# Performance work log

Hardware: AMD Instinct MI355X
Metric: run time of the kernel (lower is better)

Reference implementation:

```python
import jax, jax.numpy as jnp
import numpy as np

TAU = 1.0      # temperature for gumbel-softmax
EPS = 1e-12    # F.normalize eps


def _l2norm(v, axis):
    n = jnp.sqrt(jnp.sum(v * v, axis=axis, keepdims=True))
    return v / jnp.maximum(n, EPS)


def setup_inputs() -> dict:
    key = jax.random.key(0)
    k1, k2, k3, k4 = jax.random.split(key, 4)
    b, c, h, w, n = 8, 512, 64, 64, 1024
    x = jax.random.normal(k1, (b, c, h, w), dtype=jnp.float32)
    centers = jax.random.normal(k2, (n, c), dtype=jnp.float32)          # VQ codebook
    clusters = jax.random.normal(k3, (n, c), dtype=jnp.float32)         # ClusterLookup param
    gumbel_noise = jax.random.gumbel(k4, (b, n, h, w), dtype=jnp.float32)
    return {"x": x, "centers": centers, "clusters": clusters, "gumbel_noise": gumbel_noise}


def reference(x, centers, clusters, gumbel_noise):
    # similarity logits: [b, n, h, w]
    inner = jnp.einsum('bchw,nc->bnhw', x, centers)
    # hard gumbel-softmax (straight-through) over code dim
    y_soft = jax.nn.softmax((inner + gumbel_noise) / TAU, axis=1)
    idx = jnp.argmax(y_soft, axis=1)                                     # [b, h, w]
    y_hard = jax.nn.one_hot(idx, centers.shape[0], axis=1, dtype=y_soft.dtype)
    one_hot = y_hard - jax.lax.stop_gradient(y_soft) + y_soft            # [b, n, h, w]
    # quantized features: codebook lookup expressed as einsum
    z_q = jnp.einsum('bnhw,nd->bdhw', one_hot, centers)                  # [b, c, h, w]
    # ClusterLookup(z_q, alpha=None, is_direct=False)
    nf = _l2norm(z_q, axis=1)
    ncl = _l2norm(clusters, axis=1)
    ip = jnp.einsum('bchw,nc->bnhw', nf, ncl)                            # cluster logits
    preds = jnp.argmax(ip, axis=1)                                       # [b, h, w] int
    probs = jax.nn.one_hot(preds, clusters.shape[0], axis=1, dtype=ip.dtype)
    cluster_loss = -jnp.mean(jnp.sum(probs * ip, axis=1))
    return (cluster_loss, preds, ip, z_q)
```

## Files before the change

### kernel.cpp

```cpp
#include <hip/hip_runtime.h>
#include <math.h>

#define C 512
#define HW 4096
#define N 1024
#define NPIX 32768
#define MARGIN 2.0f

typedef short s16x8 __attribute__((ext_vector_type(8)));
typedef float f32x4 __attribute__((ext_vector_type(4)));

__device__ inline unsigned short f2bf(float f) {
    unsigned int u = __float_as_uint(f);
    return (unsigned short)((u + 0x7FFFu + ((u >> 16) & 1u)) >> 16);
}
__device__ inline float h2f(unsigned short u) {
    _Float16 h; __builtin_memcpy(&h, &u, 2); return (float)h;
}
__device__ inline unsigned short f2h(float f) {
    _Float16 h = (_Float16)f; unsigned short u; __builtin_memcpy(&u, &h, 2); return u;
}
__device__ inline unsigned int mono(float v) {
    unsigned int u = __float_as_uint(v);
    return (u & 0x80000000u) ? ~u : (u | 0x80000000u);
}

__global__ __launch_bounds__(64) void k_norms(const float* __restrict__ centers,
                                              const float* __restrict__ clusters,
                                              float* __restrict__ cnorm,
                                              float* __restrict__ clnorm) {
    int r = blockIdx.x;
    const float* src = (r < N) ? (centers + (size_t)r * C) : (clusters + (size_t)(r - N) * C);
    int lane = threadIdx.x;
    float s = 0.f;
    for (int k = lane; k < C; k += 64) { float v = src[k]; s += v * v; }
    #pragma unroll
    for (int m = 1; m < 64; m <<= 1) s += __shfl_xor(s, m, 64);
    if (lane == 0) {
        float nrm = sqrtf(s);
        if (nrm < 1e-12f) nrm = 1e-12f;
        if (r < N) cnorm[r] = nrm; else clnorm[r - N] = nrm;
    }
}

__global__ __launch_bounds__(256) void k_gemmM(const float* __restrict__ centers,
                                               const float* __restrict__ clusters,
                                               const float* __restrict__ cnorm,
                                               const float* __restrict__ clnorm,
                                               float* __restrict__ M) {
    __shared__ float as[32][68];
    __shared__ float bs[32][68];
    int tid = threadIdx.x;
    int tx = tid & 15, ty = tid >> 4;
    int i0 = blockIdx.x * 64, j0 = blockIdx.y * 64;
    int lrow = tid >> 2, lkq = (tid & 3) * 8;
    float acc[4][4] = {};
    for (int kc = 0; kc < C; kc += 32) {
        float4 a0 = *(const float4*)(centers + (size_t)(i0 + lrow) * C + kc + lkq);
        float4 a1 = *(const float4*)(centers + (size_t)(i0 + lrow) * C + kc + lkq + 4);
        float4 b0 = *(const float4*)(clusters + (size_t)(j0 + lrow) * C + kc + lkq);
        float4 b1 = *(const float4*)(clusters + (size_t)(j0 + lrow) * C + kc + lkq + 4);
        __syncthreads();
        as[lkq+0][lrow]=a0.x; as[lkq+1][lrow]=a0.y; as[lkq+2][lrow]=a0.z; as[lkq+3][lrow]=a0.w;
        as[lkq+4][lrow]=a1.x; as[lkq+5][lrow]=a1.y; as[lkq+6][lrow]=a1.z; as[lkq+7][lrow]=a1.w;
        bs[lkq+0][lrow]=b0.x; bs[lkq+1][lrow]=b0.y; bs[lkq+2][lrow]=b0.z; bs[lkq+3][lrow]=b0.w;
        bs[lkq+4][lrow]=b1.x; bs[lkq+5][lrow]=b1.y; bs[lkq+6][lrow]=b1.z; bs[lkq+7][lrow]=b1.w;
        __syncthreads();
        #pragma unroll
        for (int k = 0; k < 32; k += 4) {
            float av[4][4], bv[4][4];
            #pragma unroll
            for (int kk = 0; kk < 4; ++kk) {
                float4 ta = *(const float4*)&as[k+kk][tx*4];
                float4 tb = *(const float4*)&bs[k+kk][ty*4];
                av[kk][0]=ta.x; av[kk][1]=ta.y; av[kk][2]=ta.z; av[kk][3]=ta.w;
                bv[kk][0]=tb.x; bv[kk][1]=tb.y; bv[kk][2]=tb.z; bv[kk][3]=tb.w;
            }
            #pragma unroll
            for (int kk = 0; kk < 4; ++kk)
                #pragma unroll
                for (int ii = 0; ii < 4; ++ii)
                    #pragma unroll
                    for (int jj = 0; jj < 4; ++jj)
                        acc[ii][jj] = fmaf(av[kk][ii], bv[kk][jj], acc[ii][jj]);
        }
    }
    float rci[4], rcj[4];
    #pragma unroll
    for (int ii = 0; ii < 4; ++ii) rci[ii] = cnorm[i0 + tx*4 + ii];
    #pragma unroll
    for (int jj = 0; jj < 4; ++jj) rcj[jj] = clnorm[j0 + ty*4 + jj];
    #pragma unroll
    for (int ii = 0; ii < 4; ++ii)
        #pragma unroll
        for (int jj = 0; jj < 4; ++jj)
            M[(size_t)(i0 + tx*4 + ii) * N + (j0 + ty*4 + jj)] = acc[ii][jj] / (rci[ii] * rcj[jj]);
}

__global__ __launch_bounds__(256) void k_rowstat(const float* __restrict__ M,
                                                 float* __restrict__ rowmax,
                                                 int* __restrict__ rowarg) {
    __shared__ float sv[256];
    __shared__ int   sa[256];
    int i = blockIdx.x, tid = threadIdx.x;
    float bv = -INFINITY; int ba = 0;
    for (int j = tid; j < N; j += 256) {
        float v = M[(size_t)i * N + j];
        if (v > bv || (v == bv && j < ba)) { bv = v; ba = j; }
    }
    sv[tid] = bv; sa[tid] = ba;
    __syncthreads();
    for (int s = 128; s > 0; s >>= 1) {
        if (tid < s) {
            float v = sv[tid + s]; int a = sa[tid + s];
            if (v > sv[tid] || (v == sv[tid] && a < sa[tid])) { sv[tid] = v; sa[tid] = a; }
        }
        __syncthreads();
    }
    if (tid == 0) { rowmax[i] = sv[0]; rowarg[i] = sa[0]; }
}

__global__ __launch_bounds__(256) void k_prepT(const float* __restrict__ x,
                                               float* __restrict__ xT) {
    __shared__ float t[64][65];
    int bidx = blockIdx.x;
    int pt = bidx & 63, kt = (bidx >> 6) & 7, b = bidx >> 9;
    int r = threadIdx.x >> 4, c4 = (threadIdx.x & 15) * 4;
    const float* src = x + ((size_t)b * C + kt * 64) * HW + pt * 64;
    #pragma unroll
    for (int rr = 0; rr < 4; ++rr) {
        int row = rr * 16 + r;
        float4 v = *(const float4*)(src + (size_t)row * HW + c4);
        t[row][c4] = v.x; t[row][c4+1] = v.y; t[row][c4+2] = v.z; t[row][c4+3] = v.w;
    }
    __syncthreads();
    float* dst = xT + ((size_t)b * HW + pt * 64) * C + kt * 64;
    #pragma unroll
    for (int rr = 0; rr < 4; ++rr) {
        int row = rr * 16 + r;
        float4 v = { t[c4][row], t[c4+1][row], t[c4+2][row], t[c4+3][row] };
        *(float4*)(dst + (size_t)row * C + c4) = v;
    }
}

__global__ __launch_bounds__(64) void k_cenfrag(const float* __restrict__ centers,
                                                unsigned short* __restrict__ cenB) {
    int f = blockIdx.x;
    int nt = f >> 4, kt = f & 15;
    int lane = threadIdx.x;
    int r = lane & 15, g = lane >> 4;
    const float* src = centers + (size_t)(nt * 16 + r) * C + kt * 32 + g * 4;
    float4 lo = *(const float4*)src;
    float4 hi = *(const float4*)(src + 16);
    union { unsigned short us[8]; uint4 q; } u;
    u.us[0]=f2bf(lo.x); u.us[1]=f2bf(lo.y); u.us[2]=f2bf(lo.z); u.us[3]=f2bf(lo.w);
    u.us[4]=f2bf(hi.x); u.us[5]=f2bf(hi.y); u.us[6]=f2bf(hi.z); u.us[7]=f2bf(hi.w);
    *(uint4*)(cenB + ((size_t)f * 64 + lane) * 8) = u.q;
}

__global__ __launch_bounds__(512, 4) void k_fused(const float* __restrict__ xT,
                                                  const unsigned short* __restrict__ cenB,
                                                  const float* __restrict__ gumbel,
                                                  const float* __restrict__ centers,
                                                  int* __restrict__ idxb) {
    __shared__ uint4 cen4[2][2][1024];
    __shared__ unsigned long long pixkey[64];
    __shared__ unsigned int candlist[8][256];
    __shared__ int candcount[8];

    int tid = threadIdx.x;
    int lane = tid & 63, w = tid >> 6;
    int r = lane & 15, g = lane >> 4;
    int pt = w & 3, gr = w >> 2;

    int p0 = blockIdx.x * 64;
    int b = p0 >> 12, hw0 = p0 & (HW - 1);

    if (tid < 64) pixkey[tid] = 0ull;
    if (tid < 8) candcount[tid] = 0;

    s16x8 a[16];
    {
        const float* xrow = xT + (size_t)(p0 + pt * 16 + r) * C;
        #pragma unroll
        for (int kt = 0; kt < 16; ++kt) {
            float4 lo = *(const float4*)(xrow + kt * 32 + g * 4);
            float4 hi = *(const float4*)(xrow + kt * 32 + 16 + g * 4);
            s16x8 t;
            t[0]=(short)f2bf(lo.x); t[1]=(short)f2bf(lo.y); t[2]=(short)f2bf(lo.z); t[3]=(short)f2bf(lo.w);
            t[4]=(short)f2bf(hi.x); t[5]=(short)f2bf(hi.y); t[6]=(short)f2bf(hi.z); t[7]=(short)f2bf(hi.w);
            a[kt] = t;
        }
    }

    const uint4* cb = (const uint4*)cenB;
    {
        const uint4* src = cb + (size_t)(gr * 32) * 1024 + pt * 256 + lane;
        uint4* dst = &cen4[gr][0][pt * 256 + lane];
        #pragma unroll
        for (int i = 0; i < 4; ++i) dst[i * 64] = src[i * 64];
    }
    __syncthreads();

    float m4[4] = {-INFINITY, -INFINITY, -INFINITY, -INFINITY};
    int cur = 0;
    const float* gpx = gumbel + (size_t)b * N * HW + hw0 + pt * 16 + g * 4;

    for (int tc = 0; tc < 8; ++tc) {
        unsigned int keepH[8];
        #pragma unroll
        for (int s = 0; s < 4; ++s) {
            int t = tc * 4 + s;
            int tn = t + 1;
            uint4 cr0, cr1, cr2, cr3;
            if (tn < 32) {
                const uint4* src = cb + (size_t)(gr * 32 + tn) * 1024 + pt * 256 + lane;
                cr0 = src[0]; cr1 = src[64]; cr2 = src[128]; cr3 = src[192];
            }
            float4 gv = *(const float4*)(gpx + (size_t)((gr * 32 + t) * 16 + r) * HW);
            const s16x8* bp = (const s16x8*)&cen4[gr][cur][0] + lane;
            f32x4 acc0 = {0.f,0.f,0.f,0.f}, acc1 = {0.f,0.f,0.f,0.f};
            #pragma unroll
            for (int kt = 0; kt < 16; kt += 2) {
                acc0 = __builtin_amdgcn_mfma_f32_16x16x32_bf16(a[kt],   bp[kt*64],     acc0, 0,0,0);
                acc1 = __builtin_amdgcn_mfma_f32_16x16x32_bf16(a[kt+1], bp[(kt+1)*64], acc1, 0,0,0);
            }
            float v0 = acc0[0]+acc1[0]+gv.x, v1 = acc0[1]+acc1[1]+gv.y;
            float v2 = acc0[2]+acc1[2]+gv.z, v3 = acc0[3]+acc1[3]+gv.w;
            m4[0]=fmaxf(m4[0],v0); m4[1]=fmaxf(m4[1],v1);
            m4[2]=fmaxf(m4[2],v2); m4[3]=fmaxf(m4[3],v3);
            keepH[s*2]   = (unsigned int)f2h(v0) | ((unsigned int)f2h(v1) << 16);
            keepH[s*2+1] = (unsigned int)f2h(v2) | ((unsigned int)f2h(v3) << 16);
            if (tn < 32) {
                uint4* dst = &cen4[gr][cur ^ 1][pt * 256 + lane];
                dst[0] = cr0; dst[64] = cr1; dst[128] = cr2; dst[192] = cr3;
            }
            __syncthreads();
            cur ^= 1;
        }
        #pragma unroll
        for (int s2 = 1; s2 < 16; s2 <<= 1) {
            #pragma unroll
            for (int j = 0; j < 4; ++j) m4[j] = fmaxf(m4[j], __shfl_xor(m4[j], s2, 64));
        }
        float thr[4];
        #pragma unroll
        for (int j = 0; j < 4; ++j) thr[j] = m4[j] - MARGIN;
        #pragma unroll
        for (int s = 0; s < 4; ++s) {
            int nn = ((gr * 32 + tc * 4 + s) << 4) + r;
            #pragma unroll
            for (int j2 = 0; j2 < 2; ++j2) {
                unsigned int pk = keepH[s * 2 + j2];
                float lo = h2f((unsigned short)(pk & 0xFFFFu));
                float hi = h2f((unsigned short)(pk >> 16));
                if (lo >= thr[j2 * 2]) {
                    int pos = atomicAdd(&candcount[w], 1);
                    if (pos < 256) candlist[w][pos] =
                        (unsigned int)nn | ((unsigned int)(pt * 16 + g * 4 + j2 * 2) << 10);
                }
                if (hi >= thr[j2 * 2 + 1]) {
                    int pos = atomicAdd(&candcount[w], 1);
                    if (pos < 256) candlist[w][pos] =
                        (unsigned int)nn | ((unsigned int)(pt * 16 + g * 4 + j2 * 2 + 1) << 10);
                }
            }
        }
    }

    int cc = candcount[w]; if (cc > 256) cc = 256;
    int sl = lane & 15, cg = lane >> 4;
    for (int t0 = 0; t0 < cc; t0 += 4) {
        int c = t0 + cg;
        bool valid = c < cc;
        unsigned int e = candlist[w][valid ? c : 0];
        int n = (int)(e & 1023u), pl = (int)(e >> 10);
        const float* xr = xT + (size_t)(p0 + pl) * C;
        const float* cenr = centers + (size_t)n * C;
        float s = 0.f;
        #pragma unroll
        for (int m = 0; m < 8; ++m) {
            int G = sl + (m << 4);
            float4 xv = *(const float4*)(xr + (G << 2));
            float4 cv = *(const float4*)(cenr + (G << 2));
            s = fmaf(xv.x, cv.x, s); s = fmaf(xv.y, cv.y, s);
            s = fmaf(xv.z, cv.z, s); s = fmaf(xv.w, cv.w, s);
        }
        #pragma unroll
        for (int s2 = 1; s2 < 16; s2 <<= 1) s += __shfl_xor(s, s2, 64);
        if (valid && sl == 0) {
            float val = s + gumbel[((size_t)b * N + n) * HW + hw0 + pl];
            unsigned long long key = ((unsigned long long)mono(val) << 32) | (unsigned int)(1023 - n);
            atomicMax(&pixkey[pl], key);
        }
    }
    __syncthreads();
    if (tid < 64) idxb[p0 + tid] = 1023 - (int)(unsigned int)(pixkey[tid] & 0xFFFFFFFFull);
}

__global__ __launch_bounds__(256) void k_preds(const int* __restrict__ idxb,
                                               const float* __restrict__ rowmax,
                                               const int* __restrict__ rowarg,
                                               float* __restrict__ preds_out,
                                               float* __restrict__ partial) {
    __shared__ float sv[256];
    int gid = blockIdx.x * 256 + threadIdx.x;
    int i = idxb[gid];
    preds_out[gid] = (float)rowarg[i];
    sv[threadIdx.x] = rowmax[i];
    __syncthreads();
    for (int s = 128; s > 0; s >>= 1) {
        if (threadIdx.x < s) sv[threadIdx.x] += sv[threadIdx.x + s];
        __syncthreads();
    }
    if (threadIdx.x == 0) partial[blockIdx.x] = sv[0];
}

__global__ __launch_bounds__(256) void k_gather(const float* __restrict__ src, int ncols,
                                                const int* __restrict__ idx,
                                                float* __restrict__ dst) {
    __shared__ float rows[64][65];
    int tile = blockIdx.x;
    int col0 = blockIdx.y * 64;
    int tid = threadIdx.x;
    int lane = tid & 63, w = tid >> 6;
    int b = tile >> 6, hw0 = (tile & 63) << 6;
    #pragma unroll
    for (int r8 = 0; r8 < 16; ++r8) {
        int r = w * 16 + r8;
        int row = idx[tile * 64 + r];
        rows[r][lane] = src[(size_t)row * ncols + col0 + lane];
    }
    __syncthreads();
    #pragma unroll
    for (int jj = 0; jj < 16; ++jj) {
        int j = col0 + w * 16 + jj;
        dst[((size_t)b * ncols + j) * HW + hw0 + lane] = rows[lane][w * 16 + jj];
    }
}

__global__ __launch_bounds__(128) void k_loss(const float* __restrict__ partial,
                                              float* __restrict__ out) {
    __shared__ float sv[128];
    sv[threadIdx.x] = partial[threadIdx.x];
    __syncthreads();
    for (int s = 64; s > 0; s >>= 1) {
        if (threadIdx.x < s) sv[threadIdx.x] += sv[threadIdx.x + s];
        __syncthreads();
    }
    if (threadIdx.x == 0) out[0] = -(sv[0] / 32768.0f);
}

extern "C" void kernel_launch(void* const* d_in, const int* in_sizes, int n_in,
                              void* d_out, int out_size, void* d_ws, size_t ws_size,
                              hipStream_t stream) {
    const float* x        = (const float*)d_in[0];
    const float* centers  = (const float*)d_in[1];
    const float* clusters = (const float*)d_in[2];
    const float* gumbel   = (const float*)d_in[3];
    float* out = (float*)d_out;

    char* w = (char*)d_ws;
    int*   idxb    = (int*)w;
    float* cnorm   = (float*)(w + 131072);
    float* clnorm  = cnorm + 1024;
    float* rowmax  = clnorm + 1024;
    int*   rowarg  = (int*)(rowmax + 1024);
    float* partial = (float*)(rowarg + 1024);
    float* M       = (float*)(w + 262144);
    unsigned short* cenB = (unsigned short*)(w + 4456448);

    float* out_loss  = out;
    float* out_preds = out + 1;
    float* out_ip    = out + 1 + 32768;
    float* out_zq    = out + 1 + 32768 + (size_t)N * NPIX;

    float* xT = out_zq;

    k_norms  <<<2048, 64, 0, stream>>>(centers, clusters, cnorm, clnorm);
    k_gemmM  <<<dim3(16, 16), 256, 0, stream>>>(centers, clusters, cnorm, clnorm, M);
    k_rowstat<<<1024, 256, 0, stream>>>(M, rowmax, rowarg);
    k_cenfrag<<<1024, 64, 0, stream>>>(centers, cenB);
    k_prepT  <<<4096, 256, 0, stream>>>(x, xT);
    k_fused  <<<512, 512, 0, stream>>>(xT, cenB, gumbel, centers, idxb);
    k_preds  <<<128, 256, 0, stream>>>(idxb, rowmax, rowarg, out_preds, partial);
    k_gather <<<dim3(512, 16), 256, 0, stream>>>(M, N, idxb, out_ip);
    k_gather <<<dim3(512, 8),  256, 0, stream>>>(centers, C, idxb, out_zq);
    k_loss   <<<1, 128, 0, stream>>>(partial, out_loss);
}
```

Baseline: 295.8 us.

## Stream codebook tiles into LDS with direct global_load_lds in fused kernel

```diff
diff --git a/kernel.cpp b/kernel.cpp
--- a/kernel.cpp
+++ b/kernel.cpp
@@ -23,6 +23,11 @@
 __device__ inline unsigned int mono(float v) {
     unsigned int u = __float_as_uint(v);
     return (u & 0x80000000u) ? ~u : (u | 0x80000000u);
+}
+__device__ inline void gload_lds16(const void* gsrc, void* ldst) {
+    __builtin_amdgcn_global_load_lds(
+        (const __attribute__((address_space(1))) unsigned int*)gsrc,
+        (__attribute__((address_space(3))) unsigned int*)ldst, 16, 0, 0);
 }
 
 __global__ __launch_bounds__(64) void k_norms(const float* __restrict__ centers,
@@ -158,30 +163,36 @@
     *(uint4*)(cenB + ((size_t)f * 64 + lane) * 8) = u.q;
 }
 
-__global__ __launch_bounds__(512, 4) void k_fused(const float* __restrict__ xT,
+__global__ __launch_bounds__(256, 3) void k_fused(const float* __restrict__ xT,
                                                   const unsigned short* __restrict__ cenB,
                                                   const float* __restrict__ gumbel,
                                                   const float* __restrict__ centers,
                                                   int* __restrict__ idxb) {
-    __shared__ uint4 cen4[2][2][1024];
+    __shared__ unsigned short cen[2][8192];
     __shared__ unsigned long long pixkey[64];
-    __shared__ unsigned int candlist[8][256];
-    __shared__ int candcount[8];
+    __shared__ unsigned int candlist[4][256];
+    __shared__ int candcount[4];
 
     int tid = threadIdx.x;
     int lane = tid & 63, w = tid >> 6;
     int r = lane & 15, g = lane >> 4;
-    int pt = w & 3, gr = w >> 2;
 
     int p0 = blockIdx.x * 64;
     int b = p0 >> 12, hw0 = p0 & (HW - 1);
 
     if (tid < 64) pixkey[tid] = 0ull;
-    if (tid < 8) candcount[tid] = 0;
+    if (tid < 4) candcount[tid] = 0;
+
+    {
+        const char* src = (const char*)cenB + w * 4096 + lane * 16;
+        char* dst = (char*)&cen[0][0] + w * 4096;
+        #pragma unroll
+        for (int i = 0; i < 4; ++i) gload_lds16(src + i * 1024, dst + i * 1024);
+    }
 
     s16x8 a[16];
     {
-        const float* xrow = xT + (size_t)(p0 + pt * 16 + r) * C;
+        const float* xrow = xT + (size_t)(p0 + w * 16 + r) * C;
         #pragma unroll
         for (int kt = 0; kt < 16; ++kt) {
             float4 lo = *(const float4*)(xrow + kt * 32 + g * 4);
@@ -192,33 +203,25 @@
             a[kt] = t;
         }
     }
-
-    const uint4* cb = (const uint4*)cenB;
-    {
-        const uint4* src = cb + (size_t)(gr * 32) * 1024 + pt * 256 + lane;
-        uint4* dst = &cen4[gr][0][pt * 256 + lane];
-        #pragma unroll
-        for (int i = 0; i < 4; ++i) dst[i * 64] = src[i * 64];
-    }
-    __syncthreads();
-
+    __syncthreads();
+
+    const float* gpx = gumbel + (size_t)b * N * HW + hw0 + w * 16 + g * 4;
     float m4[4] = {-INFINITY, -INFINITY, -INFINITY, -INFINITY};
     int cur = 0;
-    const float* gpx = gumbel + (size_t)b * N * HW + hw0 + pt * 16 + g * 4;
 
     for (int tc = 0; tc < 8; ++tc) {
-        unsigned int keepH[8];
-        #pragma unroll
-        for (int s = 0; s < 4; ++s) {
-            int t = tc * 4 + s;
-            int tn = t + 1;
-            uint4 cr0, cr1, cr2, cr3;
-            if (tn < 32) {
-                const uint4* src = cb + (size_t)(gr * 32 + tn) * 1024 + pt * 256 + lane;
-                cr0 = src[0]; cr1 = src[64]; cr2 = src[128]; cr3 = src[192];
+        unsigned int keepH[16];
+        #pragma unroll
+        for (int s = 0; s < 8; ++s) {
+            int t = tc * 8 + s;
+            if (t < 63) {
+                const char* src = (const char*)cenB + (size_t)(t + 1) * 16384 + w * 4096 + lane * 16;
+                char* dst = (char*)&cen[cur ^ 1][0] + w * 4096;
+                #pragma unroll
+                for (int i = 0; i < 4; ++i) gload_lds16(src + i * 1024, dst + i * 1024);
             }
-            float4 gv = *(const float4*)(gpx + (size_t)((gr * 32 + t) * 16 + r) * HW);
-            const s16x8* bp = (const s16x8*)&cen4[gr][cur][0] + lane;
+            float4 gv = *(const float4*)(gpx + (size_t)(t * 16 + r) * HW);
+            const s16x8* bp = (const s16x8*)&cen[cur][0] + lane;
             f32x4 acc0 = {0.f,0.f,0.f,0.f}, acc1 = {0.f,0.f,0.f,0.f};
             #pragma unroll
             for (int kt = 0; kt < 16; kt += 2) {
@@ -231,10 +234,6 @@
             m4[2]=fmaxf(m4[2],v2); m4[3]=fmaxf(m4[3],v3);
             keepH[s*2]   = (unsigned int)f2h(v0) | ((unsigned int)f2h(v1) << 16);
             keepH[s*2+1] = (unsigned int)f2h(v2) | ((unsigned int)f2h(v3) << 16);
-            if (tn < 32) {
-                uint4* dst = &cen4[gr][cur ^ 1][pt * 256 + lane];
-                dst[0] = cr0; dst[64] = cr1; dst[128] = cr2; dst[192] = cr3;
-            }
             __syncthreads();
             cur ^= 1;
         }
@@ -247,8 +246,8 @@
         #pragma unroll
         for (int j = 0; j < 4; ++j) thr[j] = m4[j] - MARGIN;
         #pragma unroll
-        for (int s = 0; s < 4; ++s) {
-            int nn = ((gr * 32 + tc * 4 + s) << 4) + r;
+        for (int s = 0; s < 8; ++s) {
+            int nn = ((tc * 8 + s) << 4) + r;
             #pragma unroll
             for (int j2 = 0; j2 < 2; ++j2) {
                 unsigned int pk = keepH[s * 2 + j2];
@@ -257,12 +256,12 @@
                 if (lo >= thr[j2 * 2]) {
                     int pos = atomicAdd(&candcount[w], 1);
                     if (pos < 256) candlist[w][pos] =
-                        (unsigned int)nn | ((unsigned int)(pt * 16 + g * 4 + j2 * 2) << 10);
+                        (unsigned int)nn | ((unsigned int)(w * 16 + g * 4 + j2 * 2) << 10);
                 }
                 if (hi >= thr[j2 * 2 + 1]) {
                     int pos = atomicAdd(&candcount[w], 1);
                     if (pos < 256) candlist[w][pos] =
-                        (unsigned int)nn | ((unsigned int)(pt * 16 + g * 4 + j2 * 2 + 1) << 10);
+                        (unsigned int)nn | ((unsigned int)(w * 16 + g * 4 + j2 * 2 + 1) << 10);
                 }
             }
         }
@@ -382,7 +381,7 @@
     k_rowstat<<<1024, 256, 0, stream>>>(M, rowmax, rowarg);
     k_cenfrag<<<1024, 64, 0, stream>>>(centers, cenB);
     k_prepT  <<<4096, 256, 0, stream>>>(x, xT);
-    k_fused  <<<512, 512, 0, stream>>>(xT, cenB, gumbel, centers, idxb);
+    k_fused  <<<512, 256, 0, stream>>>(xT, cenB, gumbel, centers, idxb);
     k_preds  <<<128, 256, 0, stream>>>(idxb, rowmax, rowarg, out_preds, partial);
     k_gather <<<dim3(512, 16), 256, 0, stream>>>(M, N, idxb, out_ip);
     k_gather <<<dim3(512, 8),  256, 0, stream>>>(centers, C, idxb, out_zq);
```

Result: faster. 272.3 us (-7.9%).
